# Kernel tuning notes

Measured on AMD Instinct MI355X. Metric: run time of the kernel, lower is better.

Reference implementation:

```python
import jax, jax.numpy as jnp
import numpy as np

B, S, E, H, HD, M = 2, 2048, 1024, 16, 64, 2048  # batch, seq, embed, heads, head_dim, mem_width


def setup_inputs() -> dict:
    key = jax.random.key(0)
    k1, k2, k3, k4, k5 = jax.random.split(key, 5)
    tensor = jax.random.normal(k1, (B, S, E), dtype=jnp.float32)
    # QueryProj: Linear(E -> [H, HD]) with weight + bias (kaiming-style scale)
    Wq = jax.random.normal(k2, (E, H, HD), dtype=jnp.float32) / np.sqrt(E)
    bq = jnp.zeros((H, HD), dtype=jnp.float32)
    # Learnable key/value memory banks [H, M, HD]
    K = jax.random.normal(k3, (H, M, HD), dtype=jnp.float32) / np.sqrt(HD)
    V = jax.random.normal(k4, (H, M, HD), dtype=jnp.float32) / np.sqrt(HD)
    # DeheadProj: Linear([H, HD] -> E)
    Wd = jax.random.normal(k5, (H, HD, E), dtype=jnp.float32) / np.sqrt(H * HD)
    bd = jnp.zeros((E,), dtype=jnp.float32)
    return {"tensor": tensor, "Wq": Wq, "bq": bq, "K": K, "V": V, "Wd": Wd, "bd": bd}


def reference(tensor, Wq, bq, K, V, Wd, bd):
    # Head-splitting query projection: [B,S,E] -> [B,S,H,HD]
    q = jnp.einsum('bse,ehd->bshd', tensor, Wq) + bq
    # Attention logits against fixed parameter memory: [B,S,H,M]
    logits = jnp.einsum('bshd,hmd->bshm', q, K)
    score = jax.nn.softmax(logits, axis=-1)  # mode == 'softmax'
    # Value readout, scaled AFTER the matmul by sqrt(head_dim) (as in source)
    attn = jnp.einsum('bshm,hmd->bshd', score, V) / jnp.sqrt(jnp.asarray(HD, dtype=q.dtype))
    # Dehead projection back to embedding width: [B,S,E]
    out = jnp.einsum('bshd,hde->bse', attn, Wd) + bd
    return out
```

## Files before the change

### kernel.cpp

```cpp
#include <hip/hip_runtime.h>

typedef _Float16 half8 __attribute__((ext_vector_type(8)));
typedef _Float16 half4v __attribute__((ext_vector_type(4)));
typedef __fp16 fp16x2 __attribute__((ext_vector_type(2)));
typedef float f32x4 __attribute__((ext_vector_type(4)));
typedef float f32x16 __attribute__((ext_vector_type(16)));
typedef float float4v __attribute__((ext_vector_type(4)));
typedef unsigned uint32x2 __attribute__((ext_vector_type(2)));

constexpr int NS = 4096;
constexpr int E  = 1024;
constexpr int H  = 16;
constexpr int HD = 64;
constexpr int M  = 2048;
constexpr int HE = 1024;

__device__ __forceinline__ void gload16(const _Float16* g, _Float16* l) {
  __builtin_amdgcn_global_load_lds((__attribute__((address_space(1))) void*)g,
                                   (__attribute__((address_space(3))) void*)l, 16, 0, 0);
}

__device__ __forceinline__ float fexp2(float x) {
#if __has_builtin(__builtin_amdgcn_exp2f)
  return __builtin_amdgcn_exp2f(x);
#else
  return __expf(x * 0.6931471805599453f);
#endif
}

__device__ __forceinline__ unsigned pkh(float a, float b) {
  fp16x2 t = __builtin_amdgcn_cvt_pkrtz(a, b);
  return __builtin_bit_cast(unsigned, t);
}

__device__ __forceinline__ uint32x2 pl32swap(unsigned a, unsigned b) {
#if __has_builtin(__builtin_amdgcn_permlane32_swap)
  return __builtin_amdgcn_permlane32_swap(a, b, false, false);
#else
  unsigned sa = (unsigned)__shfl_xor((int)a, 32, 64);
  unsigned sb = (unsigned)__shfl_xor((int)b, 32, 64);
  uint32x2 r;
  r.x = (threadIdx.x & 32) ? sb : a;
  r.y = (threadIdx.x & 32) ? b : sa;
  return r;
#endif
}

__device__ __forceinline__ half8 mk8(unsigned a, unsigned b, unsigned c, unsigned d) {
  union { unsigned u[4]; half8 h; } t;
  t.u[0] = a; t.u[1] = b; t.u[2] = c; t.u[3] = d;
  return t.h;
}


__global__ void cvt_f32_to_f16(const float* __restrict__ in, _Float16* __restrict__ out,
                               float scale) {
  int i = (blockIdx.x * 256 + threadIdx.x) * 4;
  float4v v = *(const float4v*)(in + i);
  half4v o = { (_Float16)(v[0] * scale), (_Float16)(v[1] * scale),
               (_Float16)(v[2] * scale), (_Float16)(v[3] * scale) };
  *(half4v*)(out + i) = o;
}

__global__ void transpose_cvt(const float* __restrict__ in, _Float16* __restrict__ out,
                              int R, int C) {
  __shared__ float tile[32][33];
  int b = blockIdx.z;
  in  += (size_t)b * R * C;
  out += (size_t)b * R * C;
  int c0 = blockIdx.x * 32, r0 = blockIdx.y * 32;
  int tx = threadIdx.x, ty = threadIdx.y;
#pragma unroll
  for (int i = 0; i < 4; ++i)
    tile[ty + 8 * i][tx] = in[(size_t)(r0 + ty + 8 * i) * C + c0 + tx];
  __syncthreads();
#pragma unroll
  for (int i = 0; i < 4; ++i)
    out[(size_t)(c0 + ty + 8 * i) * R + r0 + tx] = (_Float16)tile[tx][ty + 8 * i];
}

__global__ void transpose_cvt2(const float* __restrict__ inA, const float* __restrict__ inB,
                               _Float16* __restrict__ outA, _Float16* __restrict__ outB) {
  __shared__ float tile[32][33];
  const float* in = blockIdx.z ? inB : inA;
  _Float16* out = blockIdx.z ? outB : outA;
  int c0 = blockIdx.x * 32, r0 = blockIdx.y * 32;
  int tx = threadIdx.x, ty = threadIdx.y;
#pragma unroll
  for (int i = 0; i < 4; ++i)
    tile[ty + 8 * i][tx] = in[(size_t)(r0 + ty + 8 * i) * 1024 + c0 + tx];
  __syncthreads();
#pragma unroll
  for (int i = 0; i < 4; ++i)
    out[(size_t)(c0 + ty + 8 * i) * 1024 + r0 + tx] = (_Float16)tile[tx][ty + 8 * i];
}


template <typename OUT_T>
__global__ __launch_bounds__(512, 4) void gemm_f16(
    const _Float16* __restrict__ A,
    const _Float16* __restrict__ Bt,
    const float* __restrict__ bias,
    OUT_T* __restrict__ C,
    int Ncols, int K, float scale)
{
  __shared__ alignas(16) _Float16 Ab[2][8 * 512];
  __shared__ alignas(16) _Float16 Bb[2][4 * 512];
  const int tid = threadIdx.x;
  const int wave = tid >> 6, lane = tid & 63;
  const int l15 = lane & 15, l4 = lane >> 4;

  const int nwg = gridDim.x;
  int wg = (blockIdx.x & 7) * (nwg >> 3) + (blockIdx.x >> 3);
  const int nbn = Ncols >> 6;
  const int mblk = wg / nbn, nblk = wg % nbn;

  const _Float16* aS = A  + (size_t)(mblk * 128 + wave * 16 + l15) * K + l4 * 8;
  const _Float16* bS = Bt + (size_t)(nblk * 64 + (wave & 3) * 16 + l15) * K + l4 * 8;
  _Float16* aD0 = &Ab[0][wave * 512];
  _Float16* aD1 = &Ab[1][wave * 512];
  _Float16* bD0 = &Bb[0][(wave & 3) * 512];
  _Float16* bD1 = &Bb[1][(wave & 3) * 512];

  const int wr = wave >> 1, wc = wave & 1;
  f32x4 acc[2][2];
#pragma unroll
  for (int i = 0; i < 2; ++i)
#pragma unroll
    for (int n = 0; n < 2; ++n) acc[i][n] = (f32x4){0.f, 0.f, 0.f, 0.f};

  gload16(aS, aD0);
  if (wave < 4) gload16(bS, bD0);
  aS += 32; bS += 32;

  const int nk = K >> 5;
  for (int kt = 0; kt < nk; ++kt) {
    __syncthreads();
    if (kt + 1 < nk) {
      gload16(aS, (kt & 1) ? aD0 : aD1);
      if (wave < 4) gload16(bS, (kt & 1) ? bD0 : bD1);
      aS += 32; bS += 32;
    }
    const _Float16* Ac = (kt & 1) ? &Ab[1][0] : &Ab[0][0];
    const _Float16* Bc = (kt & 1) ? &Bb[1][0] : &Bb[0][0];
    half8 af[2], bf[2];
#pragma unroll
    for (int i = 0; i < 2; ++i) af[i] = *(const half8*)(Ac + (wr * 2 + i) * 512 + lane * 8);
#pragma unroll
    for (int n = 0; n < 2; ++n) bf[n] = *(const half8*)(Bc + (wc * 2 + n) * 512 + lane * 8);
    __builtin_amdgcn_s_setprio(1);
#pragma unroll
    for (int i = 0; i < 2; ++i)
#pragma unroll
      for (int n = 0; n < 2; ++n)
        acc[i][n] = __builtin_amdgcn_mfma_f32_16x16x32_f16(af[i], bf[n], acc[i][n], 0, 0, 0);
    __builtin_amdgcn_s_setprio(0);
  }

  const int row0 = mblk * 128 + wr * 32;
  const int col0 = nblk * 64 + wc * 32;
#pragma unroll
  for (int n = 0; n < 2; ++n) {
    int col = col0 + n * 16 + l15;
    float bv = bias[col];
#pragma unroll
    for (int i = 0; i < 2; ++i)
#pragma unroll
      for (int r = 0; r < 4; ++r) {
        int row = row0 + i * 16 + l4 * 4 + r;
        C[(size_t)row * Ncols + col] = (OUT_T)(acc[i][n][r] * scale + bv);
      }
  }
}


__global__ __launch_bounds__(256, 4) void attn_fused(
    const _Float16* __restrict__ qh,
    const _Float16* __restrict__ Kh,
    const _Float16* __restrict__ Vth,
    _Float16* __restrict__ Op0,
    _Float16* __restrict__ Op1,
    float* __restrict__ Spart)
{
  __shared__ alignas(16) _Float16 Kb[2][4096];
  __shared__ alignas(16) _Float16 Vb[2][4096];

  int wg = (blockIdx.x & 7) * 128 + (blockIdx.x >> 3);
  const int h = wg >> 6, half = (wg >> 5) & 1, sblk = wg & 31;
  const int m0 = half * 1024;
  const int tid = threadIdx.x;
  const int wave = tid >> 6, lane = tid & 63;
  const int l31 = lane & 31, hi = lane >> 5;
  const int s0 = sblk * 128 + wave * 32;

  half8 qf[4];
  {
    const _Float16* qp = qh + (size_t)(s0 + l31) * HE + h * HD + hi * 8;
    qf[0] = *(const half8*)(qp);
    qf[1] = *(const half8*)(qp + 16);
    qf[2] = *(const half8*)(qp + 32);
    qf[3] = *(const half8*)(qp + 48);
  }

  const _Float16* kS = Kh + (size_t)h * M * HD
                       + (size_t)((wave >> 1) * 32 + l31) * HD + (wave & 1) * 32 + hi * 8;
  const _Float16* vS = Vth + (size_t)(h * HD + (wave & 1) * 32 + l31) * M
                       + (wave >> 1) * 32 + hi * 8;
  const int dOff = wave * 1024 + lane * 8;

  f32x16 accA = {0.f,0.f,0.f,0.f,0.f,0.f,0.f,0.f,0.f,0.f,0.f,0.f,0.f,0.f,0.f,0.f};
  f32x16 accB = {0.f,0.f,0.f,0.f,0.f,0.f,0.f,0.f,0.f,0.f,0.f,0.f,0.f,0.f,0.f,0.f};
  float lsum = 0.f;

#define STAGE(b, mm) {                                        \
    gload16(kS + (size_t)(mm) * HD,      &Kb[b][dOff]);       \
    gload16(kS + (size_t)(mm) * HD + 16, &Kb[b][dOff + 512]); \
    gload16(vS + (mm),                   &Vb[b][dOff]);       \
    gload16(vS + (mm) + 16,              &Vb[b][dOff + 512]); }

  STAGE(0, m0);
  for (int kt = 0; kt < 16; ++kt) {
    const int cur = kt & 1;
    __syncthreads();
    if (kt < 15) STAGE(cur ^ 1, m0 + (kt + 1) * 64);

    const _Float16* Kc = &Kb[cur][0];
    const _Float16* Vc = &Vb[cur][0];
    half8 kf[8];
#pragma unroll
    for (int c = 0; c < 8; ++c) kf[c] = *(const half8*)(Kc + c * 512 + lane * 8);
    f32x16 sA = {0.f,0.f,0.f,0.f,0.f,0.f,0.f,0.f,0.f,0.f,0.f,0.f,0.f,0.f,0.f,0.f};
    f32x16 sB = sA;
    __builtin_amdgcn_s_setprio(1);
#pragma unroll
    for (int c = 0; c < 4; ++c)
      sA = __builtin_amdgcn_mfma_f32_32x32x16_f16(kf[c], qf[c], sA, 0, 0, 0);
#pragma unroll
    for (int c = 0; c < 4; ++c)
      sB = __builtin_amdgcn_mfma_f32_32x32x16_f16(kf[4 + c], qf[c], sB, 0, 0, 0);
    __builtin_amdgcn_s_setprio(0);

    unsigned pdA[8], pdB[8];
    float la = 0.f;
#pragma unroll
    for (int i = 0; i < 8; ++i) {
      float a0 = fexp2(sA[2 * i]);
      float a1 = fexp2(sA[2 * i + 1]);
      float b0 = fexp2(sB[2 * i]);
      float b1 = fexp2(sB[2 * i + 1]);
      la += (a0 + a1) + (b0 + b1);
      pdA[i] = pkh(a0, a1);
      pdB[i] = pkh(b0, b1);
    }
    lsum += la;
    uint32x2 wA0 = pl32swap(pdA[0], pdA[2]);
    uint32x2 wA1 = pl32swap(pdA[1], pdA[3]);
    uint32x2 wA2 = pl32swap(pdA[4], pdA[6]);
    uint32x2 wA3 = pl32swap(pdA[5], pdA[7]);
    half8 paA0 = mk8(wA0.x, wA1.x, wA0.y, wA1.y);
    half8 paA1 = mk8(wA2.x, wA3.x, wA2.y, wA3.y);
    uint32x2 wB0 = pl32swap(pdB[0], pdB[2]);
    uint32x2 wB1 = pl32swap(pdB[1], pdB[3]);
    uint32x2 wB2 = pl32swap(pdB[4], pdB[6]);
    uint32x2 wB3 = pl32swap(pdB[5], pdB[7]);
    half8 paB0 = mk8(wB0.x, wB1.x, wB0.y, wB1.y);
    half8 paB1 = mk8(wB2.x, wB3.x, wB2.y, wB3.y);

    {
      half8 v0 = *(const half8*)(Vc + lane * 8);
      half8 v1 = *(const half8*)(Vc + 512 + lane * 8);
      half8 v2 = *(const half8*)(Vc + 1024 + lane * 8);
      half8 v3 = *(const half8*)(Vc + 1536 + lane * 8);
      __builtin_amdgcn_s_setprio(1);
      accA = __builtin_amdgcn_mfma_f32_32x32x16_f16(paA0, v0, accA, 0, 0, 0);
      accA = __builtin_amdgcn_mfma_f32_32x32x16_f16(paA1, v1, accA, 0, 0, 0);
      accB = __builtin_amdgcn_mfma_f32_32x32x16_f16(paA0, v2, accB, 0, 0, 0);
      accB = __builtin_amdgcn_mfma_f32_32x32x16_f16(paA1, v3, accB, 0, 0, 0);
      __builtin_amdgcn_s_setprio(0);
    }
    {
      half8 v0 = *(const half8*)(Vc + 2048 + lane * 8);
      half8 v1 = *(const half8*)(Vc + 2560 + lane * 8);
      half8 v2 = *(const half8*)(Vc + 3072 + lane * 8);
      half8 v3 = *(const half8*)(Vc + 3584 + lane * 8);
      __builtin_amdgcn_s_setprio(1);
      accA = __builtin_amdgcn_mfma_f32_32x32x16_f16(paB0, v0, accA, 0, 0, 0);
      accA = __builtin_amdgcn_mfma_f32_32x32x16_f16(paB1, v1, accA, 0, 0, 0);
      accB = __builtin_amdgcn_mfma_f32_32x32x16_f16(paB0, v2, accB, 0, 0, 0);
      accB = __builtin_amdgcn_mfma_f32_32x32x16_f16(paB1, v3, accB, 0, 0, 0);
      __builtin_amdgcn_s_setprio(0);
    }
  }
#undef STAGE

  _Float16* Op = half ? Op1 : Op0;
  float* Sp = Spart + (size_t)half * (NS * H);
#pragma unroll
  for (int r = 0; r < 16; ++r) {
    int q = s0 + (r & 3) + 8 * (r >> 2) + 4 * hi;
    Op[(size_t)q * HE + h * HD + l31]      = (_Float16)accA[r];
    Op[(size_t)q * HE + h * HD + 32 + l31] = (_Float16)accB[r];
  }
  float tot = lsum + __shfl_xor(lsum, 32, 64);
  if (hi == 0) Sp[(size_t)(s0 + l31) * H + h] = tot;
}

__global__ void attn_combine(const _Float16* __restrict__ O0, const _Float16* __restrict__ O1,
                             const float* __restrict__ Spart, _Float16* __restrict__ out) {
  int idx = (blockIdx.x * 256 + threadIdx.x) * 8;
  int row = idx >> 10, he = idx & 1023, h = he >> 6;
  half8 a = *(const half8*)(O0 + idx);
  half8 b = *(const half8*)(O1 + idx);
  float s = Spart[(size_t)row * H + h] + Spart[(size_t)(NS + row) * H + h];
  float inv = 1.0f / s;
  half8 o;
#pragma unroll
  for (int j = 0; j < 8; ++j) o[j] = (_Float16)(((float)a[j] + (float)b[j]) * inv);
  *(half8*)(out + idx) = o;
}


extern "C" void kernel_launch(void* const* d_in, const int* in_sizes, int n_in,
                              void* d_out, int out_size, void* d_ws, size_t ws_size,
                              hipStream_t stream) {
  const float* tensor = (const float*)d_in[0];
  const float* Wq     = (const float*)d_in[1];
  const float* bq     = (const float*)d_in[2];
  const float* Kp     = (const float*)d_in[3];
  const float* Vp     = (const float*)d_in[4];
  const float* Wd     = (const float*)d_in[5];
  const float* bd     = (const float*)d_in[6];
  float* out = (float*)d_out;

  char* ws = (char*)d_ws;
  _Float16* th    = (_Float16*)(ws);
  _Float16* qhb   = (_Float16*)(ws + (8  << 20));
  _Float16* attnh = (_Float16*)(ws + (16 << 20));
  _Float16* Wqt   = (_Float16*)(ws + (24 << 20));
  _Float16* Wdt   = (_Float16*)(ws + (26 << 20));
  _Float16* Khb   = (_Float16*)(ws + (28 << 20));
  _Float16* Vth   = (_Float16*)(ws + (32 << 20));
  _Float16* Op0   = (_Float16*)(ws);
  _Float16* Op1   = (_Float16*)(ws + (36 << 20));
  float*    Spart = (float*)(ws + (24 << 20));

  cvt_f32_to_f16<<<(NS * E) / 1024, 256, 0, stream>>>(tensor, th, 1.0f);
  cvt_f32_to_f16<<<(H * M * HD) / 1024, 256, 0, stream>>>(Kp, Khb, 1.44269504088896f);
  transpose_cvt2<<<dim3(32, 32, 2), dim3(32, 8), 0, stream>>>(Wq, Wd, Wqt, Wdt);
  transpose_cvt<<<dim3(2, 64, 16), dim3(32, 8), 0, stream>>>(Vp, Vth, 2048, 64);

  gemm_f16<_Float16><<<512, 512, 0, stream>>>(th, Wqt, bq, qhb, HE, E, 1.0f);
  attn_fused<<<1024, 256, 0, stream>>>(qhb, Khb, Vth, Op0, Op1, Spart);
  attn_combine<<<(NS * HE) / 2048, 256, 0, stream>>>(Op0, Op1, Spart, attnh);
  gemm_f16<float><<<512, 512, 0, stream>>>(attnh, Wdt, bd, out, E, HE, 0.125f);
}
```

Baseline: 124.3 us.

## Split attention memory into quarters and retile GEMM to 64x64 blocks

The attention kernel now splits the memory dimension into four 512-wide chunks instead of two, doubling the grid to 2048 workgroups, with a four-way combine kernel that sums partial outputs and softmax denominators. The GEMM is retiled from 128x64 tiles with 512 threads to 64x64 tiles with 256 threads, using a K-step of 64 per stage. Both changes aim to raise parallelism and occupancy on the many CUs, and the launch bound on attention is raised to 5 blocks. In exchange, the combine kernel reads twice as much partial data, there are more partial writes, and workspace buffers are remapped.

```diff
diff --git a/kernel.cpp b/kernel.cpp
--- a/kernel.cpp
+++ b/kernel.cpp
@@ -97,15 +97,15 @@
 
 
 template <typename OUT_T>
-__global__ __launch_bounds__(512, 4) void gemm_f16(
+__global__ __launch_bounds__(256, 4) void gemm_f16(
     const _Float16* __restrict__ A,
     const _Float16* __restrict__ Bt,
     const float* __restrict__ bias,
     OUT_T* __restrict__ C,
     int Ncols, int K, float scale)
 {
-  __shared__ alignas(16) _Float16 Ab[2][8 * 512];
-  __shared__ alignas(16) _Float16 Bb[2][4 * 512];
+  __shared__ alignas(16) _Float16 Ab[2][4096];
+  __shared__ alignas(16) _Float16 Bb[2][4096];
   const int tid = threadIdx.x;
   const int wave = tid >> 6, lane = tid & 63;
   const int l15 = lane & 15, l4 = lane >> 4;
@@ -115,12 +115,9 @@
   const int nbn = Ncols >> 6;
   const int mblk = wg / nbn, nblk = wg % nbn;
 
-  const _Float16* aS = A  + (size_t)(mblk * 128 + wave * 16 + l15) * K + l4 * 8;
-  const _Float16* bS = Bt + (size_t)(nblk * 64 + (wave & 3) * 16 + l15) * K + l4 * 8;
-  _Float16* aD0 = &Ab[0][wave * 512];
-  _Float16* aD1 = &Ab[1][wave * 512];
-  _Float16* bD0 = &Bb[0][(wave & 3) * 512];
-  _Float16* bD1 = &Bb[1][(wave & 3) * 512];
+  const _Float16* aS = A  + (size_t)(mblk * 64 + wave * 16 + l15) * K + l4 * 8;
+  const _Float16* bS = Bt + (size_t)(nblk * 64 + wave * 16 + l15) * K + l4 * 8;
+  const int dOff = wave * 512 + lane * 8;
 
   const int wr = wave >> 1, wc = wave & 1;
   f32x4 acc[2][2];
@@ -129,35 +126,40 @@
 #pragma unroll
     for (int n = 0; n < 2; ++n) acc[i][n] = (f32x4){0.f, 0.f, 0.f, 0.f};
 
-  gload16(aS, aD0);
-  if (wave < 4) gload16(bS, bD0);
-  aS += 32; bS += 32;
-
-  const int nk = K >> 5;
+#define GSTAGE(b, kk) {                              \
+    gload16(aS + (kk),      &Ab[b][dOff]);           \
+    gload16(aS + (kk) + 32, &Ab[b][2048 + dOff]);    \
+    gload16(bS + (kk),      &Bb[b][dOff]);           \
+    gload16(bS + (kk) + 32, &Bb[b][2048 + dOff]); }
+
+  GSTAGE(0, 0);
+  const int nk = K >> 6;
   for (int kt = 0; kt < nk; ++kt) {
     __syncthreads();
-    if (kt + 1 < nk) {
-      gload16(aS, (kt & 1) ? aD0 : aD1);
-      if (wave < 4) gload16(bS, (kt & 1) ? bD0 : bD1);
-      aS += 32; bS += 32;
+    if (kt + 1 < nk) GSTAGE((kt + 1) & 1, (kt + 1) * 64);
+    const _Float16* Ac = &Ab[kt & 1][0];
+    const _Float16* Bc = &Bb[kt & 1][0];
+#pragma unroll
+    for (int ks = 0; ks < 2; ++ks) {
+      half8 af[2], bf[2];
+#pragma unroll
+      for (int i = 0; i < 2; ++i)
+        af[i] = *(const half8*)(Ac + ks * 2048 + (wr * 2 + i) * 512 + lane * 8);
+#pragma unroll
+      for (int n = 0; n < 2; ++n)
+        bf[n] = *(const half8*)(Bc + ks * 2048 + (wc * 2 + n) * 512 + lane * 8);
+      __builtin_amdgcn_s_setprio(1);
+#pragma unroll
+      for (int i = 0; i < 2; ++i)
+#pragma unroll
+        for (int n = 0; n < 2; ++n)
+          acc[i][n] = __builtin_amdgcn_mfma_f32_16x16x32_f16(af[i], bf[n], acc[i][n], 0, 0, 0);
+      __builtin_amdgcn_s_setprio(0);
     }
-    const _Float16* Ac = (kt & 1) ? &Ab[1][0] : &Ab[0][0];
-    const _Float16* Bc = (kt & 1) ? &Bb[1][0] : &Bb[0][0];
-    half8 af[2], bf[2];
-#pragma unroll
-    for (int i = 0; i < 2; ++i) af[i] = *(const half8*)(Ac + (wr * 2 + i) * 512 + lane * 8);
-#pragma unroll
-    for (int n = 0; n < 2; ++n) bf[n] = *(const half8*)(Bc + (wc * 2 + n) * 512 + lane * 8);
-    __builtin_amdgcn_s_setprio(1);
-#pragma unroll
-    for (int i = 0; i < 2; ++i)
-#pragma unroll
-      for (int n = 0; n < 2; ++n)
-        acc[i][n] = __builtin_amdgcn_mfma_f32_16x16x32_f16(af[i], bf[n], acc[i][n], 0, 0, 0);
-    __builtin_amdgcn_s_setprio(0);
-  }
-
-  const int row0 = mblk * 128 + wr * 32;
+  }
+#undef GSTAGE
+
+  const int row0 = mblk * 64 + wr * 32;
   const int col0 = nblk * 64 + wc * 32;
 #pragma unroll
   for (int n = 0; n < 2; ++n) {
@@ -174,20 +176,22 @@
 }
 
 
-__global__ __launch_bounds__(256, 4) void attn_fused(
+__global__ __launch_bounds__(256, 5) void attn_fused(
     const _Float16* __restrict__ qh,
     const _Float16* __restrict__ Kh,
     const _Float16* __restrict__ Vth,
     _Float16* __restrict__ Op0,
     _Float16* __restrict__ Op1,
+    _Float16* __restrict__ Op2,
+    _Float16* __restrict__ Op3,
     float* __restrict__ Spart)
 {
   __shared__ alignas(16) _Float16 Kb[2][4096];
   __shared__ alignas(16) _Float16 Vb[2][4096];
 
-  int wg = (blockIdx.x & 7) * 128 + (blockIdx.x >> 3);
-  const int h = wg >> 6, half = (wg >> 5) & 1, sblk = wg & 31;
-  const int m0 = half * 1024;
+  int wg = (blockIdx.x & 7) * 256 + (blockIdx.x >> 3);
+  const int h = wg >> 7, quarter = (wg >> 5) & 3, sblk = wg & 31;
+  const int m0 = quarter * 512;
   const int tid = threadIdx.x;
   const int wave = tid >> 6, lane = tid & 63;
   const int l31 = lane & 31, hi = lane >> 5;
@@ -219,10 +223,10 @@
     gload16(vS + (mm) + 16,              &Vb[b][dOff + 512]); }
 
   STAGE(0, m0);
-  for (int kt = 0; kt < 16; ++kt) {
+  for (int kt = 0; kt < 8; ++kt) {
     const int cur = kt & 1;
     __syncthreads();
-    if (kt < 15) STAGE(cur ^ 1, m0 + (kt + 1) * 64);
+    if (kt < 7) STAGE(cur ^ 1, m0 + (kt + 1) * 64);
 
     const _Float16* Kc = &Kb[cur][0];
     const _Float16* Vc = &Vb[cur][0];
@@ -293,8 +297,8 @@
   }
 #undef STAGE
 
-  _Float16* Op = half ? Op1 : Op0;
-  float* Sp = Spart + (size_t)half * (NS * H);
+  _Float16* Op = (quarter == 0) ? Op0 : (quarter == 1) ? Op1 : (quarter == 2) ? Op2 : Op3;
+  float* Sp = Spart + (size_t)quarter * (NS * H);
 #pragma unroll
   for (int r = 0; r < 16; ++r) {
     int q = s0 + (r & 3) + 8 * (r >> 2) + 4 * hi;
@@ -305,17 +309,22 @@
   if (hi == 0) Sp[(size_t)(s0 + l31) * H + h] = tot;
 }
 
-__global__ void attn_combine(const _Float16* __restrict__ O0, const _Float16* __restrict__ O1,
-                             const float* __restrict__ Spart, _Float16* __restrict__ out) {
+__global__ void attn_combine4(const _Float16* __restrict__ O0, const _Float16* __restrict__ O1,
+                              const _Float16* __restrict__ O2, const _Float16* __restrict__ O3,
+                              const float* __restrict__ Spart, _Float16* __restrict__ out) {
   int idx = (blockIdx.x * 256 + threadIdx.x) * 8;
   int row = idx >> 10, he = idx & 1023, h = he >> 6;
   half8 a = *(const half8*)(O0 + idx);
   half8 b = *(const half8*)(O1 + idx);
-  float s = Spart[(size_t)row * H + h] + Spart[(size_t)(NS + row) * H + h];
+  half8 c = *(const half8*)(O2 + idx);
+  half8 d = *(const half8*)(O3 + idx);
+  const float* sp = Spart + (size_t)row * H + h;
+  float s = sp[0] + sp[(size_t)NS * H] + sp[(size_t)2 * NS * H] + sp[(size_t)3 * NS * H];
   float inv = 1.0f / s;
   half8 o;
 #pragma unroll
-  for (int j = 0; j < 8; ++j) o[j] = (_Float16)(((float)a[j] + (float)b[j]) * inv);
+  for (int j = 0; j < 8; ++j)
+    o[j] = (_Float16)((((float)a[j] + (float)b[j]) + ((float)c[j] + (float)d[j])) * inv);
   *(half8*)(out + idx) = o;
 }
 
@@ -336,21 +345,23 @@
   _Float16* th    = (_Float16*)(ws);
   _Float16* qhb   = (_Float16*)(ws + (8  << 20));
   _Float16* attnh = (_Float16*)(ws + (16 << 20));
-  _Float16* Wqt   = (_Float16*)(ws + (24 << 20));
+  float*    Spart = (float*)(ws + (24 << 20));
   _Float16* Wdt   = (_Float16*)(ws + (26 << 20));
   _Float16* Khb   = (_Float16*)(ws + (28 << 20));
   _Float16* Vth   = (_Float16*)(ws + (32 << 20));
+  _Float16* Wqt   = (_Float16*)(ws + (36 << 20));
   _Float16* Op0   = (_Float16*)(ws);
   _Float16* Op1   = (_Float16*)(ws + (36 << 20));
-  float*    Spart = (float*)(ws + (24 << 20));
+  _Float16* Op2   = (_Float16*)(ws + (44 << 20));
+  _Float16* Op3   = (_Float16*)(ws + (52 << 20));
 
   cvt_f32_to_f16<<<(NS * E) / 1024, 256, 0, stream>>>(tensor, th, 1.0f);
   cvt_f32_to_f16<<<(H * M * HD) / 1024, 256, 0, stream>>>(Kp, Khb, 1.44269504088896f);
   transpose_cvt2<<<dim3(32, 32, 2), dim3(32, 8), 0, stream>>>(Wq, Wd, Wqt, Wdt);
   transpose_cvt<<<dim3(2, 64, 16), dim3(32, 8), 0, stream>>>(Vp, Vth, 2048, 64);
 
-  gemm_f16<_Float16><<<512, 512, 0, stream>>>(th, Wqt, bq, qhb, HE, E, 1.0f);
-  attn_fused<<<1024, 256, 0, stream>>>(qhb, Khb, Vth, Op0, Op1, Spart);
-  attn_combine<<<(NS * HE) / 2048, 256, 0, stream>>>(Op0, Op1, Spart, attnh);
-  gemm_f16<float><<<512, 512, 0, stream>>>(attnh, Wdt, bd, out, E, HE, 0.125f);
-}
+  gemm_f16<_Float16><<<1024, 256, 0, stream>>>(th, Wqt, bq, qhb, HE, E, 1.0f);
+  attn_fused<<<2048, 256, 0, stream>>>(qhb, Khb, Vth, Op0, Op1, Op2, Op3, Spart);
+  attn_combine4<<<(NS * HE) / 2048, 256, 0, stream>>>(Op0, Op1, Op2, Op3, Spart, attnh);
+  gemm_f16<float><<<1024, 256, 0, stream>>>(attnh, Wdt, bd, out, E, HE, 0.125f);
+}
```

After: 453.5 us. +264.8%, slower.

## Triple-buffer LDS staging with explicit vmcnt waits in GEMM and attention

Applied to the files above, without the earlier changes.

Both the f16 GEMM and the fused attention kernel move from double to triple buffering of their LDS tiles. Each loop iteration now issues the load two tiles ahead and waits with hand-written s_waitcnt vmcnt counts plus a raw s_barrier, instead of a full __syncthreads before each load. The aim is to hide more global-to-LDS latency behind the MFMA work. The cost is more LDS per block: 48KB for attention, which may reduce how many blocks fit per CU. The hand-counted vmcnt values also tie correctness to exactly how many loads each wave issues.

```diff
diff --git a/kernel.cpp b/kernel.cpp
--- a/kernel.cpp
+++ b/kernel.cpp
@@ -104,8 +104,8 @@
     OUT_T* __restrict__ C,
     int Ncols, int K, float scale)
 {
-  __shared__ alignas(16) _Float16 Ab[2][8 * 512];
-  __shared__ alignas(16) _Float16 Bb[2][4 * 512];
+  __shared__ alignas(16) _Float16 Ab[3][4096];
+  __shared__ alignas(16) _Float16 Bb[3][2048];
   const int tid = threadIdx.x;
   const int wave = tid >> 6, lane = tid & 63;
   const int l15 = lane & 15, l4 = lane >> 4;
@@ -117,10 +117,6 @@
 
   const _Float16* aS = A  + (size_t)(mblk * 128 + wave * 16 + l15) * K + l4 * 8;
   const _Float16* bS = Bt + (size_t)(nblk * 64 + (wave & 3) * 16 + l15) * K + l4 * 8;
-  _Float16* aD0 = &Ab[0][wave * 512];
-  _Float16* aD1 = &Ab[1][wave * 512];
-  _Float16* bD0 = &Bb[0][(wave & 3) * 512];
-  _Float16* bD1 = &Bb[1][(wave & 3) * 512];
 
   const int wr = wave >> 1, wc = wave & 1;
   f32x4 acc[2][2];
@@ -129,20 +125,27 @@
 #pragma unroll
     for (int n = 0; n < 2; ++n) acc[i][n] = (f32x4){0.f, 0.f, 0.f, 0.f};
 
-  gload16(aS, aD0);
-  if (wave < 4) gload16(bS, bD0);
-  aS += 32; bS += 32;
+#define GSTAGE(b, kt_) {                                        \
+    gload16(aS + (kt_) * 32, &Ab[b][wave * 512]);               \
+    if (wave < 4) gload16(bS + (kt_) * 32, &Bb[b][wave * 512]); }
+
+  GSTAGE(0, 0);
+  GSTAGE(1, 1);
 
   const int nk = K >> 5;
   for (int kt = 0; kt < nk; ++kt) {
-    __syncthreads();
-    if (kt + 1 < nk) {
-      gload16(aS, (kt & 1) ? aD0 : aD1);
-      if (wave < 4) gload16(bS, (kt & 1) ? bD0 : bD1);
-      aS += 32; bS += 32;
+    if (kt < nk - 1) {
+      if (wave < 4) { asm volatile("s_waitcnt vmcnt(2)" ::: "memory"); }
+      else          { asm volatile("s_waitcnt vmcnt(1)" ::: "memory"); }
+    } else {
+      asm volatile("s_waitcnt vmcnt(0)" ::: "memory");
     }
-    const _Float16* Ac = (kt & 1) ? &Ab[1][0] : &Ab[0][0];
-    const _Float16* Bc = (kt & 1) ? &Bb[1][0] : &Bb[0][0];
+    __builtin_amdgcn_s_barrier();
+    __builtin_amdgcn_sched_barrier(0);
+    if (kt + 2 < nk) GSTAGE((kt + 2) % 3, kt + 2);
+    const int bufc = kt % 3;
+    const _Float16* Ac = &Ab[bufc][0];
+    const _Float16* Bc = &Bb[bufc][0];
     half8 af[2], bf[2];
 #pragma unroll
     for (int i = 0; i < 2; ++i) af[i] = *(const half8*)(Ac + (wr * 2 + i) * 512 + lane * 8);
@@ -156,6 +159,7 @@
         acc[i][n] = __builtin_amdgcn_mfma_f32_16x16x32_f16(af[i], bf[n], acc[i][n], 0, 0, 0);
     __builtin_amdgcn_s_setprio(0);
   }
+#undef GSTAGE
 
   const int row0 = mblk * 128 + wr * 32;
   const int col0 = nblk * 64 + wc * 32;
@@ -182,8 +186,8 @@
     _Float16* __restrict__ Op1,
     float* __restrict__ Spart)
 {
-  __shared__ alignas(16) _Float16 Kb[2][4096];
-  __shared__ alignas(16) _Float16 Vb[2][4096];
+  __shared__ alignas(16) _Float16 Kb[3][4096];
+  __shared__ alignas(16) _Float16 Vb[3][4096];
 
   int wg = (blockIdx.x & 7) * 128 + (blockIdx.x >> 3);
   const int h = wg >> 6, half = (wg >> 5) & 1, sblk = wg & 31;
@@ -206,26 +210,30 @@
                        + (size_t)((wave >> 1) * 32 + l31) * HD + (wave & 1) * 32 + hi * 8;
   const _Float16* vS = Vth + (size_t)(h * HD + (wave & 1) * 32 + l31) * M
                        + (wave >> 1) * 32 + hi * 8;
-  const int dOff = wave * 1024 + lane * 8;
+  const int dOff = wave * 1024;
 
   f32x16 accA = {0.f,0.f,0.f,0.f,0.f,0.f,0.f,0.f,0.f,0.f,0.f,0.f,0.f,0.f,0.f,0.f};
   f32x16 accB = {0.f,0.f,0.f,0.f,0.f,0.f,0.f,0.f,0.f,0.f,0.f,0.f,0.f,0.f,0.f,0.f};
   float lsum = 0.f;
 
-#define STAGE(b, mm) {                                        \
-    gload16(kS + (size_t)(mm) * HD,      &Kb[b][dOff]);       \
-    gload16(kS + (size_t)(mm) * HD + 16, &Kb[b][dOff + 512]); \
-    gload16(vS + (mm),                   &Vb[b][dOff]);       \
+#define STAGE(b, mm) {                                         \
+    gload16(kS + (size_t)(mm) * HD,      &Kb[b][dOff]);        \
+    gload16(kS + (size_t)(mm) * HD + 16, &Kb[b][dOff + 512]);  \
+    gload16(vS + (mm),                   &Vb[b][dOff]);        \
     gload16(vS + (mm) + 16,              &Vb[b][dOff + 512]); }
 
   STAGE(0, m0);
+  STAGE(1, m0 + 64);
   for (int kt = 0; kt < 16; ++kt) {
-    const int cur = kt & 1;
-    __syncthreads();
-    if (kt < 15) STAGE(cur ^ 1, m0 + (kt + 1) * 64);
-
-    const _Float16* Kc = &Kb[cur][0];
-    const _Float16* Vc = &Vb[cur][0];
+    if (kt < 15) { asm volatile("s_waitcnt vmcnt(4)" ::: "memory"); }
+    else         { asm volatile("s_waitcnt vmcnt(0)" ::: "memory"); }
+    __builtin_amdgcn_s_barrier();
+    __builtin_amdgcn_sched_barrier(0);
+    if (kt + 2 < 16) STAGE((kt + 2) % 3, m0 + (kt + 2) * 64);
+
+    const int bufc = kt % 3;
+    const _Float16* Kc = &Kb[bufc][0];
+    const _Float16* Vc = &Vb[bufc][0];
     half8 kf[8];
 #pragma unroll
     for (int c = 0; c < 8; ++c) kf[c] = *(const half8*)(Kc + c * 512 + lane * 8);
```

After: 134.4 us. +8.1%, slower.

## Double per-wave work in GEMM and attention kernels to reuse staged tiles

Applied to the files above, without the earlier changes.

The GEMM now runs with 256 threads per block instead of 512. Each wave computes a 64x32 tile instead of 32x32, and every wave loads two A rows and one B row. The attention kernel gives each wave two 32-query groups, so each staged K/V tile is reused across 64 queries. That halves the grid and halves the total K/V traffic. The cost is more accumulator registers, shown by the attention launch bound dropping from 4 to 2 blocks per CU, and fewer blocks to hide latency.

```diff
diff --git a/kernel.cpp b/kernel.cpp
--- a/kernel.cpp
+++ b/kernel.cpp
@@ -97,7 +97,7 @@
 
 
 template <typename OUT_T>
-__global__ __launch_bounds__(512, 4) void gemm_f16(
+__global__ __launch_bounds__(256, 4) void gemm_f16(
     const _Float16* __restrict__ A,
     const _Float16* __restrict__ Bt,
     const float* __restrict__ bias,
@@ -115,56 +115,61 @@
   const int nbn = Ncols >> 6;
   const int mblk = wg / nbn, nblk = wg % nbn;
 
-  const _Float16* aS = A  + (size_t)(mblk * 128 + wave * 16 + l15) * K + l4 * 8;
-  const _Float16* bS = Bt + (size_t)(nblk * 64 + (wave & 3) * 16 + l15) * K + l4 * 8;
-  _Float16* aD0 = &Ab[0][wave * 512];
-  _Float16* aD1 = &Ab[1][wave * 512];
-  _Float16* bD0 = &Bb[0][(wave & 3) * 512];
-  _Float16* bD1 = &Bb[1][(wave & 3) * 512];
+  const _Float16* aS0 = A  + (size_t)(mblk * 128 + wave * 16 + l15) * K + l4 * 8;
+  const _Float16* aS1 = aS0 + (size_t)64 * K;
+  const _Float16* bS  = Bt + (size_t)(nblk * 64 + wave * 16 + l15) * K + l4 * 8;
+  _Float16* aD0a = &Ab[0][wave * 512];
+  _Float16* aD0b = &Ab[0][(wave + 4) * 512];
+  _Float16* aD1a = &Ab[1][wave * 512];
+  _Float16* aD1b = &Ab[1][(wave + 4) * 512];
+  _Float16* bD0  = &Bb[0][wave * 512];
+  _Float16* bD1  = &Bb[1][wave * 512];
 
   const int wr = wave >> 1, wc = wave & 1;
-  f32x4 acc[2][2];
-#pragma unroll
-  for (int i = 0; i < 2; ++i)
+  f32x4 acc[4][2];
+#pragma unroll
+  for (int i = 0; i < 4; ++i)
 #pragma unroll
     for (int n = 0; n < 2; ++n) acc[i][n] = (f32x4){0.f, 0.f, 0.f, 0.f};
 
-  gload16(aS, aD0);
-  if (wave < 4) gload16(bS, bD0);
-  aS += 32; bS += 32;
+  gload16(aS0, aD0a);
+  gload16(aS1, aD0b);
+  gload16(bS, bD0);
+  aS0 += 32; aS1 += 32; bS += 32;
 
   const int nk = K >> 5;
   for (int kt = 0; kt < nk; ++kt) {
     __syncthreads();
     if (kt + 1 < nk) {
-      gload16(aS, (kt & 1) ? aD0 : aD1);
-      if (wave < 4) gload16(bS, (kt & 1) ? bD0 : bD1);
-      aS += 32; bS += 32;
+      gload16(aS0, (kt & 1) ? aD0a : aD1a);
+      gload16(aS1, (kt & 1) ? aD0b : aD1b);
+      gload16(bS,  (kt & 1) ? bD0  : bD1);
+      aS0 += 32; aS1 += 32; bS += 32;
     }
     const _Float16* Ac = (kt & 1) ? &Ab[1][0] : &Ab[0][0];
     const _Float16* Bc = (kt & 1) ? &Bb[1][0] : &Bb[0][0];
-    half8 af[2], bf[2];
-#pragma unroll
-    for (int i = 0; i < 2; ++i) af[i] = *(const half8*)(Ac + (wr * 2 + i) * 512 + lane * 8);
+    half8 af[4], bf[2];
+#pragma unroll
+    for (int i = 0; i < 4; ++i) af[i] = *(const half8*)(Ac + (wr * 4 + i) * 512 + lane * 8);
 #pragma unroll
     for (int n = 0; n < 2; ++n) bf[n] = *(const half8*)(Bc + (wc * 2 + n) * 512 + lane * 8);
     __builtin_amdgcn_s_setprio(1);
 #pragma unroll
-    for (int i = 0; i < 2; ++i)
+    for (int i = 0; i < 4; ++i)
 #pragma unroll
       for (int n = 0; n < 2; ++n)
         acc[i][n] = __builtin_amdgcn_mfma_f32_16x16x32_f16(af[i], bf[n], acc[i][n], 0, 0, 0);
     __builtin_amdgcn_s_setprio(0);
   }
 
-  const int row0 = mblk * 128 + wr * 32;
+  const int row0 = mblk * 128 + wr * 64;
   const int col0 = nblk * 64 + wc * 32;
 #pragma unroll
   for (int n = 0; n < 2; ++n) {
     int col = col0 + n * 16 + l15;
     float bv = bias[col];
 #pragma unroll
-    for (int i = 0; i < 2; ++i)
+    for (int i = 0; i < 4; ++i)
 #pragma unroll
       for (int r = 0; r < 4; ++r) {
         int row = row0 + i * 16 + l4 * 4 + r;
@@ -174,7 +179,7 @@
 }
 
 
-__global__ __launch_bounds__(256, 4) void attn_fused(
+__global__ __launch_bounds__(256, 2) void attn_fused(
     const _Float16* __restrict__ qh,
     const _Float16* __restrict__ Kh,
     const _Float16* __restrict__ Vth,
@@ -185,21 +190,22 @@
   __shared__ alignas(16) _Float16 Kb[2][4096];
   __shared__ alignas(16) _Float16 Vb[2][4096];
 
-  int wg = (blockIdx.x & 7) * 128 + (blockIdx.x >> 3);
-  const int h = wg >> 6, half = (wg >> 5) & 1, sblk = wg & 31;
+  int wg = (blockIdx.x & 7) * 64 + (blockIdx.x >> 3);
+  const int h = wg >> 5, half = (wg >> 4) & 1, qblk = wg & 15;
   const int m0 = half * 1024;
   const int tid = threadIdx.x;
   const int wave = tid >> 6, lane = tid & 63;
   const int l31 = lane & 31, hi = lane >> 5;
-  const int s0 = sblk * 128 + wave * 32;
-
-  half8 qf[4];
-  {
-    const _Float16* qp = qh + (size_t)(s0 + l31) * HE + h * HD + hi * 8;
-    qf[0] = *(const half8*)(qp);
-    qf[1] = *(const half8*)(qp + 16);
-    qf[2] = *(const half8*)(qp + 32);
-    qf[3] = *(const half8*)(qp + 48);
+  const int s0 = qblk * 256 + wave * 64;
+
+  half8 qf[2][4];
+#pragma unroll
+  for (int g = 0; g < 2; ++g) {
+    const _Float16* qp = qh + (size_t)(s0 + g * 32 + l31) * HE + h * HD + hi * 8;
+    qf[g][0] = *(const half8*)(qp);
+    qf[g][1] = *(const half8*)(qp + 16);
+    qf[g][2] = *(const half8*)(qp + 32);
+    qf[g][3] = *(const half8*)(qp + 48);
   }
 
   const _Float16* kS = Kh + (size_t)h * M * HD
@@ -208,9 +214,13 @@
                        + (wave >> 1) * 32 + hi * 8;
   const int dOff = wave * 1024 + lane * 8;
 
-  f32x16 accA = {0.f,0.f,0.f,0.f,0.f,0.f,0.f,0.f,0.f,0.f,0.f,0.f,0.f,0.f,0.f,0.f};
-  f32x16 accB = {0.f,0.f,0.f,0.f,0.f,0.f,0.f,0.f,0.f,0.f,0.f,0.f,0.f,0.f,0.f,0.f};
-  float lsum = 0.f;
+  f32x16 accA[2], accB[2];
+  float lsum[2] = {0.f, 0.f};
+#pragma unroll
+  for (int g = 0; g < 2; ++g) {
+    accA[g] = (f32x16){0.f,0.f,0.f,0.f,0.f,0.f,0.f,0.f,0.f,0.f,0.f,0.f,0.f,0.f,0.f,0.f};
+    accB[g] = (f32x16){0.f,0.f,0.f,0.f,0.f,0.f,0.f,0.f,0.f,0.f,0.f,0.f,0.f,0.f,0.f,0.f};
+  }
 
 #define STAGE(b, mm) {                                        \
     gload16(kS + (size_t)(mm) * HD,      &Kb[b][dOff]);       \
@@ -229,42 +239,47 @@
     half8 kf[8];
 #pragma unroll
     for (int c = 0; c < 8; ++c) kf[c] = *(const half8*)(Kc + c * 512 + lane * 8);
-    f32x16 sA = {0.f,0.f,0.f,0.f,0.f,0.f,0.f,0.f,0.f,0.f,0.f,0.f,0.f,0.f,0.f,0.f};
-    f32x16 sB = sA;
-    __builtin_amdgcn_s_setprio(1);
-#pragma unroll
-    for (int c = 0; c < 4; ++c)
-      sA = __builtin_amdgcn_mfma_f32_32x32x16_f16(kf[c], qf[c], sA, 0, 0, 0);
-#pragma unroll
-    for (int c = 0; c < 4; ++c)
-      sB = __builtin_amdgcn_mfma_f32_32x32x16_f16(kf[4 + c], qf[c], sB, 0, 0, 0);
-    __builtin_amdgcn_s_setprio(0);
-
-    unsigned pdA[8], pdB[8];
-    float la = 0.f;
-#pragma unroll
-    for (int i = 0; i < 8; ++i) {
-      float a0 = fexp2(sA[2 * i]);
-      float a1 = fexp2(sA[2 * i + 1]);
-      float b0 = fexp2(sB[2 * i]);
-      float b1 = fexp2(sB[2 * i + 1]);
-      la += (a0 + a1) + (b0 + b1);
-      pdA[i] = pkh(a0, a1);
-      pdB[i] = pkh(b0, b1);
-    }
-    lsum += la;
-    uint32x2 wA0 = pl32swap(pdA[0], pdA[2]);
-    uint32x2 wA1 = pl32swap(pdA[1], pdA[3]);
-    uint32x2 wA2 = pl32swap(pdA[4], pdA[6]);
-    uint32x2 wA3 = pl32swap(pdA[5], pdA[7]);
-    half8 paA0 = mk8(wA0.x, wA1.x, wA0.y, wA1.y);
-    half8 paA1 = mk8(wA2.x, wA3.x, wA2.y, wA3.y);
-    uint32x2 wB0 = pl32swap(pdB[0], pdB[2]);
-    uint32x2 wB1 = pl32swap(pdB[1], pdB[3]);
-    uint32x2 wB2 = pl32swap(pdB[4], pdB[6]);
-    uint32x2 wB3 = pl32swap(pdB[5], pdB[7]);
-    half8 paB0 = mk8(wB0.x, wB1.x, wB0.y, wB1.y);
-    half8 paB1 = mk8(wB2.x, wB3.x, wB2.y, wB3.y);
+
+    half8 paA0[2], paA1[2], paB0[2], paB1[2];
+#pragma unroll
+    for (int g = 0; g < 2; ++g) {
+      f32x16 sA = (f32x16){0.f,0.f,0.f,0.f,0.f,0.f,0.f,0.f,0.f,0.f,0.f,0.f,0.f,0.f,0.f,0.f};
+      f32x16 sB = sA;
+      __builtin_amdgcn_s_setprio(1);
+#pragma unroll
+      for (int c = 0; c < 4; ++c)
+        sA = __builtin_amdgcn_mfma_f32_32x32x16_f16(kf[c], qf[g][c], sA, 0, 0, 0);
+#pragma unroll
+      for (int c = 0; c < 4; ++c)
+        sB = __builtin_amdgcn_mfma_f32_32x32x16_f16(kf[4 + c], qf[g][c], sB, 0, 0, 0);
+      __builtin_amdgcn_s_setprio(0);
+
+      unsigned pdA[8], pdB[8];
+      float la = 0.f;
+#pragma unroll
+      for (int i = 0; i < 8; ++i) {
+        float a0 = fexp2(sA[2 * i]);
+        float a1 = fexp2(sA[2 * i + 1]);
+        float b0 = fexp2(sB[2 * i]);
+        float b1 = fexp2(sB[2 * i + 1]);
+        la += (a0 + a1) + (b0 + b1);
+        pdA[i] = pkh(a0, a1);
+        pdB[i] = pkh(b0, b1);
+      }
+      lsum[g] += la;
+      uint32x2 wA0 = pl32swap(pdA[0], pdA[2]);
+      uint32x2 wA1 = pl32swap(pdA[1], pdA[3]);
+      uint32x2 wA2 = pl32swap(pdA[4], pdA[6]);
+      uint32x2 wA3 = pl32swap(pdA[5], pdA[7]);
+      paA0[g] = mk8(wA0.x, wA1.x, wA0.y, wA1.y);
+      paA1[g] = mk8(wA2.x, wA3.x, wA2.y, wA3.y);
+      uint32x2 wB0 = pl32swap(pdB[0], pdB[2]);
+      uint32x2 wB1 = pl32swap(pdB[1], pdB[3]);
+      uint32x2 wB2 = pl32swap(pdB[4], pdB[6]);
+      uint32x2 wB3 = pl32swap(pdB[5], pdB[7]);
+      paB0[g] = mk8(wB0.x, wB1.x, wB0.y, wB1.y);
+      paB1[g] = mk8(wB2.x, wB3.x, wB2.y, wB3.y);
+    }
 
     {
       half8 v0 = *(const half8*)(Vc + lane * 8);
@@ -272,10 +287,13 @@
       half8 v2 = *(const half8*)(Vc + 1024 + lane * 8);
       half8 v3 = *(const half8*)(Vc + 1536 + lane * 8);
       __builtin_amdgcn_s_setprio(1);
-      accA = __builtin_amdgcn_mfma_f32_32x32x16_f16(paA0, v0, accA, 0, 0, 0);
-      accA = __builtin_amdgcn_mfma_f32_32x32x16_f16(paA1, v1, accA, 0, 0, 0);
-      accB = __builtin_amdgcn_mfma_f32_32x32x16_f16(paA0, v2, accB, 0, 0, 0);
-      accB = __builtin_amdgcn_mfma_f32_32x32x16_f16(paA1, v3, accB, 0, 0, 0);
+#pragma unroll
+      for (int g = 0; g < 2; ++g) {
+        accA[g] = __builtin_amdgcn_mfma_f32_32x32x16_f16(paA0[g], v0, accA[g], 0, 0, 0);
+        accA[g] = __builtin_amdgcn_mfma_f32_32x32x16_f16(paA1[g], v1, accA[g], 0, 0, 0);
+        accB[g] = __builtin_amdgcn_mfma_f32_32x32x16_f16(paA0[g], v2, accB[g], 0, 0, 0);
+        accB[g] = __builtin_amdgcn_mfma_f32_32x32x16_f16(paA1[g], v3, accB[g], 0, 0, 0);
+      }
       __builtin_amdgcn_s_setprio(0);
     }
     {
@@ -284,10 +302,13 @@
       half8 v2 = *(const half8*)(Vc + 3072 + lane * 8);
       half8 v3 = *(const half8*)(Vc + 3584 + lane * 8);
       __builtin_amdgcn_s_setprio(1);
-      accA = __builtin_amdgcn_mfma_f32_32x32x16_f16(paB0, v0, accA, 0, 0, 0);
-      accA = __builtin_amdgcn_mfma_f32_32x32x16_f16(paB1, v1, accA, 0, 0, 0);
-      accB = __builtin_amdgcn_mfma_f32_32x32x16_f16(paB0, v2, accB, 0, 0, 0);
-      accB = __builtin_amdgcn_mfma_f32_32x32x16_f16(paB1, v3, accB, 0, 0, 0);
+#pragma unroll
+      for (int g = 0; g < 2; ++g) {
+        accA[g] = __builtin_amdgcn_mfma_f32_32x32x16_f16(paB0[g], v0, accA[g], 0, 0, 0);
+        accA[g] = __builtin_amdgcn_mfma_f32_32x32x16_f16(paB1[g], v1, accA[g], 0, 0, 0);
+        accB[g] = __builtin_amdgcn_mfma_f32_32x32x16_f16(paB0[g], v2, accB[g], 0, 0, 0);
+        accB[g] = __builtin_amdgcn_mfma_f32_32x32x16_f16(paB1[g], v3, accB[g], 0, 0, 0);
+      }
       __builtin_amdgcn_s_setprio(0);
     }
   }
@@ -296,13 +317,16 @@
   _Float16* Op = half ? Op1 : Op0;
   float* Sp = Spart + (size_t)half * (NS * H);
 #pragma unroll
-  for (int r = 0; r < 16; ++r) {
-    int q = s0 + (r & 3) + 8 * (r >> 2) + 4 * hi;
-    Op[(size_t)q * HE + h * HD + l31]      = (_Float16)accA[r];
-    Op[(size_t)q * HE + h * HD + 32 + l31] = (_Float16)accB[r];
-  }
-  float tot = lsum + __shfl_xor(lsum, 32, 64);
-  if (hi == 0) Sp[(size_t)(s0 + l31) * H + h] = tot;
+  for (int g = 0; g < 2; ++g) {
+#pragma unroll
+    for (int r = 0; r < 16; ++r) {
+      int q = s0 + g * 32 + (r & 3) + 8 * (r >> 2) + 4 * hi;
+      Op[(size_t)q * HE + h * HD + l31]      = (_Float16)accA[g][r];
+      Op[(size_t)q * HE + h * HD + 32 + l31] = (_Float16)accB[g][r];
+    }
+    float tot = lsum[g] + __shfl_xor(lsum[g], 32, 64);
+    if (hi == 0) Sp[(size_t)(s0 + g * 32 + l31) * H + h] = tot;
+  }
 }
 
 __global__ void attn_combine(const _Float16* __restrict__ O0, const _Float16* __restrict__ O1,
@@ -349,8 +373,8 @@
   transpose_cvt2<<<dim3(32, 32, 2), dim3(32, 8), 0, stream>>>(Wq, Wd, Wqt, Wdt);
   transpose_cvt<<<dim3(2, 64, 16), dim3(32, 8), 0, stream>>>(Vp, Vth, 2048, 64);
 
-  gemm_f16<_Float16><<<512, 512, 0, stream>>>(th, Wqt, bq, qhb, HE, E, 1.0f);
-  attn_fused<<<1024, 256, 0, stream>>>(qhb, Khb, Vth, Op0, Op1, Spart);
+  gemm_f16<_Float16><<<512, 256, 0, stream>>>(th, Wqt, bq, qhb, HE, E, 1.0f);
+  attn_fused<<<512, 256, 0, stream>>>(qhb, Khb, Vth, Op0, Op1, Spart);
   attn_combine<<<(NS * HE) / 2048, 256, 0, stream>>>(Op0, Op1, Spart, attnh);
-  gemm_f16<float><<<512, 512, 0, stream>>>(attnh, Wdt, bd, out, E, HE, 0.125f);
-}
+  gemm_f16<float><<<512, 256, 0, stream>>>(attnh, Wdt, bd, out, E, HE, 0.125f);
+}
```

Result: faster. 119.6 us, median of 2 (-3.8%).
